# Optimization experiments

Hardware: AMD Instinct MI355X
Metric: run time of the kernel (lower is better)

Reference implementation:

```python
import jax, jax.numpy as jnp
import numpy as np

DIM, DEPTH, MULT = 512, 3, 4
E = 2 ** DEPTH            # 8 experts
HID = MULT * DIM          # 2048
B, S = 4, 1024


def setup_inputs() -> dict:
    key = jax.random.key(0)
    ks = jax.random.split(key, 7)
    sd = 1.0 / np.sqrt(DIM)
    sh = 1.0 / np.sqrt(HID)
    return {
        "x": jax.random.normal(ks[0], (B, S, DIM), dtype=jnp.float32),
        "rw": jax.random.normal(ks[1], (E - 1, DIM), dtype=jnp.float32) * sd,
        "rb": jax.random.normal(ks[2], (E - 1,), dtype=jnp.float32) * sd,
        "w1": jax.random.normal(ks[3], (E, DIM, HID), dtype=jnp.float32) * sd,
        "b1": jax.random.normal(ks[4], (E, HID), dtype=jnp.float32) * sd,
        "w2": jax.random.normal(ks[5], (E, HID, DIM), dtype=jnp.float32) * sh,
        "b2": jax.random.normal(ks[6], (E, DIM), dtype=jnp.float32) * sh,
    }


def _leaf_probs(flat_x, rw, rb):
    # Binary-tree soft routing: level d has 2**d routers at offset 2**d - 1.
    n_tok = flat_x.shape[0]
    leaf = jnp.ones((n_tok, 1), dtype=flat_x.dtype)
    for d in range(DEPTH):
        off, n = 2 ** d - 1, 2 ** d
        logits = flat_x @ rw[off:off + n].T + rb[off:off + n]   # [N, n]
        p = jax.nn.sigmoid(logits)
        # child probs: left = 1-p, right = p
        leaf = (leaf[:, :, None] * jnp.stack([1.0 - p, p], axis=2)).reshape(n_tok, 2 * n)
    return leaf  # [N, E]


def reference(x, rw, rb, w1, b1, w2, b2):
    b, s, dim = x.shape
    flat_x = x.reshape(b * s, dim)                               # [N, D]
    leaf_probs = _leaf_probs(flat_x, rw, rb)                     # [N, E]
    # Dense evaluation of all experts (soft-routing training path).
    h = jnp.einsum('nd,edh->neh', flat_x, w1) + b1[None]         # [N, E, H]
    h = jax.nn.gelu(h, approximate=False)                        # torch nn.GELU (erf)
    y = jnp.einsum('neh,ehd->ned', h, w2) + b2[None]             # [N, E, D]
    out = jnp.einsum('ned,ne->nd', y, leaf_probs)                # [N, D]
    return out.reshape(b, s, dim)
```

## Files before the change

kernel.cpp:

```cpp
#include <hip/hip_runtime.h>
#include <hip/hip_bf16.h>
#include <hip/hip_fp16.h>

#define DIM 512
#define HID 2048
#define NE 8
#define NTOK 4096

typedef _Float16 v8h __attribute__((ext_vector_type(8)));
typedef float v16f __attribute__((ext_vector_type(16)));

__device__ __forceinline__ void load16(const void* g, void* l) {
  __builtin_amdgcn_global_load_lds(
      (const __attribute__((address_space(1))) unsigned int*)g,
      (__attribute__((address_space(3))) unsigned int*)l, 16, 0, 0);
}

__device__ __forceinline__ float gelu_fast(float v) {
  float v2 = v * v;
  float u = v * __builtin_fmaf(0.07135481627f, v2, 1.5957691216f);
  float t = __expf(-u);
  return v * __builtin_amdgcn_rcpf(1.0f + t);
}

__global__ __launch_bounds__(256) void pre_kernel(const float* __restrict__ x,
                                                  const float* __restrict__ rw,
                                                  const float* __restrict__ rb,
                                                  const float* __restrict__ b2,
                                                  const float* __restrict__ w1,
                                                  const float* __restrict__ w2,
                                                  float* __restrict__ leaf,
                                                  _Float16* __restrict__ xh,
                                                  float* __restrict__ out,
                                                  _Float16* __restrict__ w1t,
                                                  _Float16* __restrict__ w2t) {
  __shared__ _Float16 tl[32][516];
  if (blockIdx.x < 1024) {
    const int lane = threadIdx.x & 63;
    const int wave = threadIdx.x >> 6;
    const int n = (blockIdx.x << 2) + wave;
    const float4* xv = (const float4*)(x + (size_t)n * DIM);
    const float4 x0 = xv[lane * 2], x1 = xv[lane * 2 + 1];
    v8h o;
    o[0] = (_Float16)x0.x; o[1] = (_Float16)x0.y; o[2] = (_Float16)x0.z; o[3] = (_Float16)x0.w;
    o[4] = (_Float16)x1.x; o[5] = (_Float16)x1.y; o[6] = (_Float16)x1.z; o[7] = (_Float16)x1.w;
    *(v8h*)(xh + (size_t)n * DIM + lane * 8) = o;
    float logits[7];
#pragma unroll
    for (int rr = 0; rr < 7; ++rr) {
      const float4* wv = (const float4*)(rw + rr * DIM);
      const float4 w0 = wv[lane * 2], w1v = wv[lane * 2 + 1];
      float s = x0.x * w0.x + x0.y * w0.y + x0.z * w0.z + x0.w * w0.w +
                x1.x * w1v.x + x1.y * w1v.y + x1.z * w1v.z + x1.w * w1v.w;
#pragma unroll
      for (int o2 = 32; o2; o2 >>= 1) s += __shfl_xor(s, o2, 64);
      logits[rr] = s + rb[rr];
    }
    const int eidx = lane & 7;
    const float p0 = 1.f / (1.f + __expf(-logits[0]));
    float f = ((eidx >> 2) & 1) ? p0 : 1.f - p0;
    const float p1 = 1.f / (1.f + __expf(-logits[1 + (eidx >> 2)]));
    f *= ((eidx >> 1) & 1) ? p1 : 1.f - p1;
    const float p2 = 1.f / (1.f + __expf(-logits[3 + (eidx >> 1)]));
    f *= (eidx & 1) ? p2 : 1.f - p2;
    if (lane < NE) leaf[(size_t)n * NE + lane] = f;
    float le[NE];
#pragma unroll
    for (int e = 0; e < NE; ++e) le[e] = __shfl(f, e, 64);
    float4 a0 = {0.f, 0.f, 0.f, 0.f}, a1 = {0.f, 0.f, 0.f, 0.f};
#pragma unroll
    for (int e = 0; e < NE; ++e) {
      const float4* bv = (const float4*)(b2 + (size_t)e * DIM + lane * 8);
      const float4 u0 = bv[0], u1 = bv[1];
      a0.x += le[e] * u0.x; a0.y += le[e] * u0.y; a0.z += le[e] * u0.z; a0.w += le[e] * u0.w;
      a1.x += le[e] * u1.x; a1.y += le[e] * u1.y; a1.z += le[e] * u1.z; a1.w += le[e] * u1.w;
    }
    float4* op = (float4*)(out + (size_t)n * DIM + lane * 8);
    op[0] = a0; op[1] = a1;
  } else {
    int t = blockIdx.x - 1024;
    const float* in;
    _Float16* outp;
    int C, Rk, kt, ct, e;
    if (t < 512) {
      in = w1; outp = w1t; C = HID; Rk = DIM;
      e = t >> 6; const int rem = t & 63; kt = rem & 15; ct = rem >> 4;
    } else {
      t -= 512;
      in = w2; outp = w2t; C = DIM; Rk = HID;
      e = t >> 6; kt = t & 63; ct = 0;
    }
    const int kb0 = kt << 5, cb0 = ct << 9;
    const size_t ebase = (size_t)e * Rk * C;
    const int tid = threadIdx.x;
#pragma unroll
    for (int i = 0; i < 16; ++i) {
      const int idx = (i << 8) + tid;
      const int row = idx >> 7, c4 = idx & 127;
      const float4 v = *(const float4*)(in + ebase + (size_t)(kb0 + row) * C + cb0 + (c4 << 2));
      _Float16* lp = &tl[row][c4 << 2];
      lp[0] = (_Float16)v.x; lp[1] = (_Float16)v.y; lp[2] = (_Float16)v.z; lp[3] = (_Float16)v.w;
    }
    __syncthreads();
#pragma unroll
    for (int h = 0; h < 2; ++h) {
      const int n = (h << 8) + tid;
      v8h o[4];
#pragma unroll
      for (int g = 0; g < 4; ++g)
#pragma unroll
        for (int u = 0; u < 8; ++u)
          o[g][u] = tl[(g << 3) + u][n];
      v8h* dst = (v8h*)(outp + ebase + (size_t)(cb0 + n) * Rk + kb0);
#pragma unroll
      for (int g = 0; g < 4; ++g) dst[g] = o[g];
    }
  }
}


__global__ __launch_bounds__(256, 3) void gemm1_kernel(const _Float16* __restrict__ xh,
                                                       const _Float16* __restrict__ w1t,
                                                       const float* __restrict__ b1,
                                                       const float* __restrict__ leaf,
                                                       _Float16* __restrict__ H) {
  const int bx = blockIdx.x;
  const int e = bx & 7;
  const int t = bx >> 3;
  const int mt = t & 31;
  const int nt = t >> 5;
  const int m0 = mt << 7, n0 = nt << 7;

  __shared__ alignas(16) _Float16 As[128 * 64];
  __shared__ alignas(16) _Float16 Bs[128 * 64];

  const int tid = threadIdx.x;
  const int lane = tid & 63;
  const int wave = tid >> 6;
  const int wm = wave >> 1, wn = wave & 1;
  const int c = lane & 31, h2 = lane >> 5;
  const int cx = c & 7;

  const int strow = tid >> 3;
  const int c8 = (tid & 7) ^ (strow & 7);
  const _Float16* pa[4];
  const _Float16* pb[4];
  _Float16* la[4];
  _Float16* lb[4];
#pragma unroll
  for (int i = 0; i < 4; ++i) {
    pa[i] = xh + (size_t)(m0 + strow + 32 * i) * DIM + (c8 << 3);
    la[i] = As + tid * 8 + i * 2048;
    pb[i] = w1t + ((size_t)e * HID + n0 + strow + 32 * i) * DIM + (c8 << 3);
    lb[i] = Bs + tid * 8 + i * 2048;
  }
  const _Float16* fA[2];
  const _Float16* fB[2];
#pragma unroll
  for (int i = 0; i < 2; ++i) fA[i] = As + ((wm << 6) + (i << 5) + c) * 64;
#pragma unroll
  for (int j = 0; j < 2; ++j) fB[j] = Bs + ((wn << 6) + (j << 5) + c) * 64;

  v16f acc[2][2];
#pragma unroll
  for (int i = 0; i < 2; ++i)
#pragma unroll
    for (int j = 0; j < 2; ++j)
      acc[i][j] = v16f{0.f,0.f,0.f,0.f,0.f,0.f,0.f,0.f,0.f,0.f,0.f,0.f,0.f,0.f,0.f,0.f};

#pragma unroll
  for (int kk = 0; kk < 8; ++kk) {
#pragma unroll
    for (int i = 0; i < 4; ++i) load16(pa[i] + kk * 64, la[i]);
#pragma unroll
    for (int i = 0; i < 4; ++i) load16(pb[i] + kk * 64, lb[i]);
    __syncthreads();
#pragma unroll
    for (int ks = 0; ks < 4; ++ks) {
      const int so = ((((ks << 1) + h2) ^ cx) << 3);
      v8h a[2], b[2];
#pragma unroll
      for (int i = 0; i < 2; ++i) a[i] = *(const v8h*)(fA[i] + so);
#pragma unroll
      for (int j = 0; j < 2; ++j) b[j] = *(const v8h*)(fB[j] + so);
#pragma unroll
      for (int i = 0; i < 2; ++i)
#pragma unroll
        for (int j = 0; j < 2; ++j)
          acc[i][j] = __builtin_amdgcn_mfma_f32_32x32x16_f16(a[i], b[j], acc[i][j], 0, 0, 0);
    }
    __syncthreads();
  }

  const float* b1e = b1 + (size_t)e * HID;
  _Float16* He = H + (size_t)e * NTOK * HID;
  const int colb = n0 + (wn << 6) + c;
  const float bias0 = b1e[colb];
  const float bias1 = b1e[colb + 32];
#pragma unroll
  for (int i = 0; i < 2; ++i) {
    const int rb0 = m0 + (wm << 6) + (i << 5) + (h2 << 2);
#pragma unroll
    for (int rg = 0; rg < 4; ++rg) {
#pragma unroll
      for (int rr = 0; rr < 4; ++rr) {
        const int row = rb0 + (rg << 3) + rr;
        const int reg = (rg << 2) + rr;
        const float p = leaf[(size_t)row * NE + e];
        _Float16* hp = He + (size_t)row * HID + colb;
        hp[0]  = (_Float16)(p * gelu_fast(acc[i][0][reg] + bias0));
        hp[32] = (_Float16)(p * gelu_fast(acc[i][1][reg] + bias1));
      }
    }
  }
}

__global__ __launch_bounds__(256, 3) void gemm2_kernel(const _Float16* __restrict__ H,
                                                       const _Float16* __restrict__ w2t,
                                                       float* __restrict__ out) {
  const int bx = blockIdx.x;
  const int e = bx & 7;
  const int dt = (bx >> 3) & 3;
  const int mt = bx >> 5;
  const int m0 = mt << 7, d0 = dt << 7;

  __shared__ alignas(16) _Float16 As[128 * 64];
  __shared__ alignas(16) _Float16 Bs[128 * 64];

  const int tid = threadIdx.x;
  const int lane = tid & 63;
  const int wave = tid >> 6;
  const int wm = wave >> 1, wn = wave & 1;
  const int c = lane & 31, h2 = lane >> 5;
  const int cx = c & 7;

  const int strow = tid >> 3;
  const int c8 = (tid & 7) ^ (strow & 7);
  const _Float16* pa[4];
  const _Float16* pb[4];
  _Float16* la[4];
  _Float16* lb[4];
#pragma unroll
  for (int i = 0; i < 4; ++i) {
    pa[i] = H + ((size_t)e * NTOK + m0 + strow + 32 * i) * HID + (c8 << 3);
    la[i] = As + tid * 8 + i * 2048;
    pb[i] = w2t + ((size_t)e * DIM + d0 + strow + 32 * i) * HID + (c8 << 3);
    lb[i] = Bs + tid * 8 + i * 2048;
  }
  const _Float16* fA[2];
  const _Float16* fB[2];
#pragma unroll
  for (int i = 0; i < 2; ++i) fA[i] = As + ((wm << 6) + (i << 5) + c) * 64;
#pragma unroll
  for (int j = 0; j < 2; ++j) fB[j] = Bs + ((wn << 6) + (j << 5) + c) * 64;

  v16f acc[2][2];
#pragma unroll
  for (int i = 0; i < 2; ++i)
#pragma unroll
    for (int j = 0; j < 2; ++j)
      acc[i][j] = v16f{0.f,0.f,0.f,0.f,0.f,0.f,0.f,0.f,0.f,0.f,0.f,0.f,0.f,0.f,0.f,0.f};

  for (int ko = 0; ko < 4; ++ko) {
#pragma unroll
    for (int u = 0; u < 8; ++u) {
#pragma unroll
      for (int i = 0; i < 4; ++i) load16(pa[i] + u * 64, la[i]);
#pragma unroll
      for (int i = 0; i < 4; ++i) load16(pb[i] + u * 64, lb[i]);
      __syncthreads();
#pragma unroll
      for (int ks = 0; ks < 4; ++ks) {
        const int so = ((((ks << 1) + h2) ^ cx) << 3);
        v8h a[2], b[2];
#pragma unroll
        for (int i = 0; i < 2; ++i) a[i] = *(const v8h*)(fA[i] + so);
#pragma unroll
        for (int j = 0; j < 2; ++j) b[j] = *(const v8h*)(fB[j] + so);
#pragma unroll
        for (int i = 0; i < 2; ++i)
#pragma unroll
          for (int j = 0; j < 2; ++j)
            acc[i][j] = __builtin_amdgcn_mfma_f32_32x32x16_f16(a[i], b[j], acc[i][j], 0, 0, 0);
      }
      __syncthreads();
    }
#pragma unroll
    for (int i = 0; i < 4; ++i) { pa[i] += 512; pb[i] += 512; }
  }

#pragma unroll
  for (int i = 0; i < 2; ++i) {
    const int rb0 = m0 + (wm << 6) + (i << 5) + (h2 << 2);
#pragma unroll
    for (int rg = 0; rg < 4; ++rg) {
#pragma unroll
      for (int rr = 0; rr < 4; ++rr) {
        const int row = rb0 + (rg << 3) + rr;
        const int reg = (rg << 2) + rr;
        float* op = out + (size_t)row * DIM + d0 + (wn << 6) + c;
        atomicAdd(op, acc[i][0][reg]);
        atomicAdd(op + 32, acc[i][1][reg]);
      }
    }
  }
}

extern "C" void kernel_launch(void* const* d_in, const int* in_sizes, int n_in,
                              void* d_out, int out_size, void* d_ws, size_t ws_size,
                              hipStream_t stream) {
  const float* x  = (const float*)d_in[0];
  const float* rw = (const float*)d_in[1];
  const float* rb = (const float*)d_in[2];
  const float* w1 = (const float*)d_in[3];
  const float* b1 = (const float*)d_in[4];
  const float* w2 = (const float*)d_in[5];
  const float* b2 = (const float*)d_in[6];
  float* out = (float*)d_out;

  char* ws = (char*)d_ws;
  const size_t xh_bytes   = (size_t)NTOK * DIM * 2;
  const size_t w1t_bytes  = (size_t)NE * HID * DIM * 2;
  const size_t w2t_bytes  = (size_t)NE * DIM * HID * 2;
  const size_t leaf_bytes = (size_t)NTOK * NE * 4;
  const size_t H_bytes    = (size_t)NE * NTOK * HID * 2;
  _Float16* xh   = (_Float16*)(ws);
  _Float16* w1t  = (_Float16*)(ws + xh_bytes);
  _Float16* w2t  = (_Float16*)(ws + xh_bytes + w1t_bytes);
  float*    leaf = (float*)(ws + xh_bytes + w1t_bytes + w2t_bytes);
  _Float16* Hbuf = (_Float16*)(ws + xh_bytes + w1t_bytes + w2t_bytes + leaf_bytes);
  if (ws_size < xh_bytes + w1t_bytes + w2t_bytes + leaf_bytes + H_bytes) return;

  pre_kernel<<<2048, 256, 0, stream>>>(x, rw, rb, b2, w1, w2, leaf, xh, out, w1t, w2t);
  gemm1_kernel<<<4096, 256, 0, stream>>>(xh, w1t, b1, leaf, Hbuf);
  gemm2_kernel<<<1024, 256, 0, stream>>>(Hbuf, w2t, out);
}
```

Before: 340.7 us.

## Double-buffer GEMM LDS tiles and split routing from weight transpose

Both GEMM kernels now use two LDS buffers: the global-to-LDS loads for the next K-slice are issued before the MFMAs on the current slice, with one barrier per step instead of two. This is meant to hide load latency behind compute. MFMA sections are bracketed by s_setprio, and occupancy hints drop from 3 to 2 blocks per SM because LDS use doubles. The pre-kernel is split into a routing kernel and a separate weight-transpose kernel, which uses a transposed LDS layout with 4-row float4 reads and vectorised half stores; this adds one kernel launch.

```diff
diff --git a/kernel.cpp b/kernel.cpp
--- a/kernel.cpp
+++ b/kernel.cpp
@@ -8,6 +8,7 @@
 #define NTOK 4096
 
 typedef _Float16 v8h __attribute__((ext_vector_type(8)));
+typedef _Float16 v4h __attribute__((ext_vector_type(4)));
 typedef float v16f __attribute__((ext_vector_type(16)));
 
 __device__ __forceinline__ void load16(const void* g, void* l) {
@@ -23,103 +24,152 @@
   return v * __builtin_amdgcn_rcpf(1.0f + t);
 }
 
-__global__ __launch_bounds__(256) void pre_kernel(const float* __restrict__ x,
-                                                  const float* __restrict__ rw,
-                                                  const float* __restrict__ rb,
-                                                  const float* __restrict__ b2,
-                                                  const float* __restrict__ w1,
-                                                  const float* __restrict__ w2,
-                                                  float* __restrict__ leaf,
-                                                  _Float16* __restrict__ xh,
-                                                  float* __restrict__ out,
-                                                  _Float16* __restrict__ w1t,
-                                                  _Float16* __restrict__ w2t) {
-  __shared__ _Float16 tl[32][516];
-  if (blockIdx.x < 1024) {
-    const int lane = threadIdx.x & 63;
-    const int wave = threadIdx.x >> 6;
-    const int n = (blockIdx.x << 2) + wave;
-    const float4* xv = (const float4*)(x + (size_t)n * DIM);
-    const float4 x0 = xv[lane * 2], x1 = xv[lane * 2 + 1];
-    v8h o;
-    o[0] = (_Float16)x0.x; o[1] = (_Float16)x0.y; o[2] = (_Float16)x0.z; o[3] = (_Float16)x0.w;
-    o[4] = (_Float16)x1.x; o[5] = (_Float16)x1.y; o[6] = (_Float16)x1.z; o[7] = (_Float16)x1.w;
-    *(v8h*)(xh + (size_t)n * DIM + lane * 8) = o;
-    float logits[7];
-#pragma unroll
-    for (int rr = 0; rr < 7; ++rr) {
-      const float4* wv = (const float4*)(rw + rr * DIM);
-      const float4 w0 = wv[lane * 2], w1v = wv[lane * 2 + 1];
-      float s = x0.x * w0.x + x0.y * w0.y + x0.z * w0.z + x0.w * w0.w +
-                x1.x * w1v.x + x1.y * w1v.y + x1.z * w1v.z + x1.w * w1v.w;
-#pragma unroll
-      for (int o2 = 32; o2; o2 >>= 1) s += __shfl_xor(s, o2, 64);
-      logits[rr] = s + rb[rr];
-    }
-    const int eidx = lane & 7;
-    const float p0 = 1.f / (1.f + __expf(-logits[0]));
-    float f = ((eidx >> 2) & 1) ? p0 : 1.f - p0;
-    const float p1 = 1.f / (1.f + __expf(-logits[1 + (eidx >> 2)]));
-    f *= ((eidx >> 1) & 1) ? p1 : 1.f - p1;
-    const float p2 = 1.f / (1.f + __expf(-logits[3 + (eidx >> 1)]));
-    f *= (eidx & 1) ? p2 : 1.f - p2;
-    if (lane < NE) leaf[(size_t)n * NE + lane] = f;
-    float le[NE];
-#pragma unroll
-    for (int e = 0; e < NE; ++e) le[e] = __shfl(f, e, 64);
-    float4 a0 = {0.f, 0.f, 0.f, 0.f}, a1 = {0.f, 0.f, 0.f, 0.f};
-#pragma unroll
-    for (int e = 0; e < NE; ++e) {
-      const float4* bv = (const float4*)(b2 + (size_t)e * DIM + lane * 8);
-      const float4 u0 = bv[0], u1 = bv[1];
-      a0.x += le[e] * u0.x; a0.y += le[e] * u0.y; a0.z += le[e] * u0.z; a0.w += le[e] * u0.w;
-      a1.x += le[e] * u1.x; a1.y += le[e] * u1.y; a1.z += le[e] * u1.z; a1.w += le[e] * u1.w;
-    }
-    float4* op = (float4*)(out + (size_t)n * DIM + lane * 8);
-    op[0] = a0; op[1] = a1;
+__global__ __launch_bounds__(256) void route_kernel(const float* __restrict__ x,
+                                                    const float* __restrict__ rw,
+                                                    const float* __restrict__ rb,
+                                                    const float* __restrict__ b2,
+                                                    float* __restrict__ leaf,
+                                                    _Float16* __restrict__ xh,
+                                                    float* __restrict__ out) {
+  const int lane = threadIdx.x & 63;
+  const int wave = threadIdx.x >> 6;
+  const int n = (blockIdx.x << 2) + wave;
+  const float4* xv = (const float4*)(x + (size_t)n * DIM);
+  const float4 x0 = xv[lane * 2], x1 = xv[lane * 2 + 1];
+  v8h o;
+  o[0] = (_Float16)x0.x; o[1] = (_Float16)x0.y; o[2] = (_Float16)x0.z; o[3] = (_Float16)x0.w;
+  o[4] = (_Float16)x1.x; o[5] = (_Float16)x1.y; o[6] = (_Float16)x1.z; o[7] = (_Float16)x1.w;
+  *(v8h*)(xh + (size_t)n * DIM + lane * 8) = o;
+  float logits[7];
+#pragma unroll
+  for (int rr = 0; rr < 7; ++rr) {
+    const float4* wv = (const float4*)(rw + rr * DIM);
+    const float4 w0 = wv[lane * 2], w1v = wv[lane * 2 + 1];
+    float s = x0.x * w0.x + x0.y * w0.y + x0.z * w0.z + x0.w * w0.w +
+              x1.x * w1v.x + x1.y * w1v.y + x1.z * w1v.z + x1.w * w1v.w;
+#pragma unroll
+    for (int o2 = 32; o2; o2 >>= 1) s += __shfl_xor(s, o2, 64);
+    logits[rr] = s + rb[rr];
+  }
+  const int eidx = lane & 7;
+  const float p0 = 1.f / (1.f + __expf(-logits[0]));
+  float f = ((eidx >> 2) & 1) ? p0 : 1.f - p0;
+  const float p1 = 1.f / (1.f + __expf(-logits[1 + (eidx >> 2)]));
+  f *= ((eidx >> 1) & 1) ? p1 : 1.f - p1;
+  const float p2 = 1.f / (1.f + __expf(-logits[3 + (eidx >> 1)]));
+  f *= (eidx & 1) ? p2 : 1.f - p2;
+  if (lane < NE) leaf[(size_t)n * NE + lane] = f;
+  float le[NE];
+#pragma unroll
+  for (int e = 0; e < NE; ++e) le[e] = __shfl(f, e, 64);
+  float4 a0 = {0.f, 0.f, 0.f, 0.f}, a1 = {0.f, 0.f, 0.f, 0.f};
+#pragma unroll
+  for (int e = 0; e < NE; ++e) {
+    const float4* bv = (const float4*)(b2 + (size_t)e * DIM + lane * 8);
+    const float4 u0 = bv[0], u1 = bv[1];
+    a0.x += le[e] * u0.x; a0.y += le[e] * u0.y; a0.z += le[e] * u0.z; a0.w += le[e] * u0.w;
+    a1.x += le[e] * u1.x; a1.y += le[e] * u1.y; a1.z += le[e] * u1.z; a1.w += le[e] * u1.w;
+  }
+  float4* op = (float4*)(out + (size_t)n * DIM + lane * 8);
+  op[0] = a0; op[1] = a1;
+}
+
+__global__ __launch_bounds__(256) void trans_kernel(const float* __restrict__ w1,
+                                                    const float* __restrict__ w2,
+                                                    _Float16* __restrict__ w1t,
+                                                    _Float16* __restrict__ w2t) {
+  __shared__ _Float16 tlT[256][36];
+  int b = blockIdx.x;
+  const float* in;
+  _Float16* outp;
+  int C, Rk, kt, ct, e;
+  if (b < 1024) {
+    in = w1; outp = w1t; C = HID; Rk = DIM;
+    e = b >> 7; const int rem = b & 127; kt = rem & 15; ct = rem >> 4;
   } else {
-    int t = blockIdx.x - 1024;
-    const float* in;
-    _Float16* outp;
-    int C, Rk, kt, ct, e;
-    if (t < 512) {
-      in = w1; outp = w1t; C = HID; Rk = DIM;
-      e = t >> 6; const int rem = t & 63; kt = rem & 15; ct = rem >> 4;
-    } else {
-      t -= 512;
-      in = w2; outp = w2t; C = DIM; Rk = HID;
-      e = t >> 6; kt = t & 63; ct = 0;
-    }
-    const int kb0 = kt << 5, cb0 = ct << 9;
-    const size_t ebase = (size_t)e * Rk * C;
-    const int tid = threadIdx.x;
-#pragma unroll
-    for (int i = 0; i < 16; ++i) {
-      const int idx = (i << 8) + tid;
-      const int row = idx >> 7, c4 = idx & 127;
-      const float4 v = *(const float4*)(in + ebase + (size_t)(kb0 + row) * C + cb0 + (c4 << 2));
-      _Float16* lp = &tl[row][c4 << 2];
-      lp[0] = (_Float16)v.x; lp[1] = (_Float16)v.y; lp[2] = (_Float16)v.z; lp[3] = (_Float16)v.w;
-    }
-    __syncthreads();
-#pragma unroll
-    for (int h = 0; h < 2; ++h) {
-      const int n = (h << 8) + tid;
-      v8h o[4];
-#pragma unroll
-      for (int g = 0; g < 4; ++g)
-#pragma unroll
-        for (int u = 0; u < 8; ++u)
-          o[g][u] = tl[(g << 3) + u][n];
-      v8h* dst = (v8h*)(outp + ebase + (size_t)(cb0 + n) * Rk + kb0);
-#pragma unroll
-      for (int g = 0; g < 4; ++g) dst[g] = o[g];
-    }
-  }
-}
-
-
-__global__ __launch_bounds__(256, 3) void gemm1_kernel(const _Float16* __restrict__ xh,
+    b -= 1024;
+    in = w2; outp = w2t; C = DIM; Rk = HID;
+    e = b >> 7; const int rem = b & 127; kt = rem & 63; ct = rem >> 6;
+  }
+  const int k0 = kt << 5, c0 = ct << 8;
+  const size_t ebase = (size_t)e * Rk * C;
+  const int tid = threadIdx.x;
+#pragma unroll
+  for (int it = 0; it < 2; ++it) {
+    const int mb = (it << 8) + tid;
+    const int rg = mb >> 6, cq = mb & 63;
+    const float* sp = in + ebase + (size_t)(k0 + (rg << 2)) * C + c0 + (cq << 2);
+    const float4 r0 = *(const float4*)(sp);
+    const float4 r1 = *(const float4*)(sp + C);
+    const float4 r2 = *(const float4*)(sp + 2 * C);
+    const float4 r3 = *(const float4*)(sp + 3 * C);
+    const int cc = cq << 2, rr = rg << 2;
+    v4h t0 = {(_Float16)r0.x, (_Float16)r1.x, (_Float16)r2.x, (_Float16)r3.x};
+    v4h t1 = {(_Float16)r0.y, (_Float16)r1.y, (_Float16)r2.y, (_Float16)r3.y};
+    v4h t2 = {(_Float16)r0.z, (_Float16)r1.z, (_Float16)r2.z, (_Float16)r3.z};
+    v4h t3 = {(_Float16)r0.w, (_Float16)r1.w, (_Float16)r2.w, (_Float16)r3.w};
+    *(v4h*)&tlT[cc + 0][rr] = t0;
+    *(v4h*)&tlT[cc + 1][rr] = t1;
+    *(v4h*)&tlT[cc + 2][rr] = t2;
+    *(v4h*)&tlT[cc + 3][rr] = t3;
+  }
+  __syncthreads();
+  v8h ov[4];
+#pragma unroll
+  for (int g = 0; g < 4; ++g) {
+    const v4h lo = *(const v4h*)&tlT[tid][g * 8];
+    const v4h hi = *(const v4h*)&tlT[tid][g * 8 + 4];
+    ov[g][0] = lo[0]; ov[g][1] = lo[1]; ov[g][2] = lo[2]; ov[g][3] = lo[3];
+    ov[g][4] = hi[0]; ov[g][5] = hi[1]; ov[g][6] = hi[2]; ov[g][7] = hi[3];
+  }
+  _Float16* dp = outp + ebase + (size_t)(c0 + tid) * Rk + k0;
+#pragma unroll
+  for (int g = 0; g < 4; ++g) *(v8h*)(dp + g * 8) = ov[g];
+}
+
+
+#define WAIT0() asm volatile("s_waitcnt vmcnt(0)" ::: "memory")
+#define BARF()                                                                \
+  {                                                                           \
+    __builtin_amdgcn_s_barrier();                                             \
+    asm volatile("" ::: "memory");                                            \
+  }
+
+#define GSTAGE(BOF, KO)                                                       \
+  {                                                                           \
+    _Pragma("unroll") for (int i = 0; i < 4; ++i)                             \
+        load16(pa[i] + (KO), la[i] + (BOF));                                  \
+    _Pragma("unroll") for (int i = 0; i < 4; ++i)                             \
+        load16(pb[i] + (KO), lb[i] + (BOF));                                  \
+  }
+
+#define GCOMPUTE(BOF)                                                         \
+  {                                                                           \
+    v8h a[2][4], b[2][4];                                                     \
+    _Pragma("unroll") for (int ks = 0; ks < 4; ++ks) {                        \
+      const int so = (BOF) + ((((ks << 1) + h2) ^ cx) << 3);                  \
+      a[0][ks] = *(const v8h*)(fA[0] + so);                                   \
+      a[1][ks] = *(const v8h*)(fA[1] + so);                                   \
+      b[0][ks] = *(const v8h*)(fB[0] + so);                                   \
+      b[1][ks] = *(const v8h*)(fB[1] + so);                                   \
+    }                                                                         \
+    __builtin_amdgcn_s_setprio(1);                                            \
+    _Pragma("unroll") for (int ks = 0; ks < 4; ++ks)                          \
+      _Pragma("unroll") for (int i = 0; i < 2; ++i)                           \
+        _Pragma("unroll") for (int j = 0; j < 2; ++j)                         \
+          acc[i][j] = __builtin_amdgcn_mfma_f32_32x32x16_f16(a[i][ks], b[j][ks], acc[i][j], 0, 0, 0); \
+    __builtin_amdgcn_s_setprio(0);                                            \
+  }
+
+#define GITER(BUFC, BUFS, KO)                                                 \
+  {                                                                           \
+    GSTAGE(BUFS, KO);                                                         \
+    GCOMPUTE(BUFC);                                                           \
+    WAIT0();                                                                  \
+    BARF();                                                                   \
+  }
+
+__global__ __launch_bounds__(256, 2) void gemm1_kernel(const _Float16* __restrict__ xh,
                                                        const _Float16* __restrict__ w1t,
                                                        const float* __restrict__ b1,
                                                        const float* __restrict__ leaf,
@@ -131,8 +181,8 @@
   const int nt = t >> 5;
   const int m0 = mt << 7, n0 = nt << 7;
 
-  __shared__ alignas(16) _Float16 As[128 * 64];
-  __shared__ alignas(16) _Float16 Bs[128 * 64];
+  __shared__ alignas(16) _Float16 As[2 * 128 * 64];
+  __shared__ alignas(16) _Float16 Bs[2 * 128 * 64];
 
   const int tid = threadIdx.x;
   const int lane = tid & 63;
@@ -168,29 +218,16 @@
     for (int j = 0; j < 2; ++j)
       acc[i][j] = v16f{0.f,0.f,0.f,0.f,0.f,0.f,0.f,0.f,0.f,0.f,0.f,0.f,0.f,0.f,0.f,0.f};
 
-#pragma unroll
-  for (int kk = 0; kk < 8; ++kk) {
-#pragma unroll
-    for (int i = 0; i < 4; ++i) load16(pa[i] + kk * 64, la[i]);
-#pragma unroll
-    for (int i = 0; i < 4; ++i) load16(pb[i] + kk * 64, lb[i]);
-    __syncthreads();
-#pragma unroll
-    for (int ks = 0; ks < 4; ++ks) {
-      const int so = ((((ks << 1) + h2) ^ cx) << 3);
-      v8h a[2], b[2];
-#pragma unroll
-      for (int i = 0; i < 2; ++i) a[i] = *(const v8h*)(fA[i] + so);
-#pragma unroll
-      for (int j = 0; j < 2; ++j) b[j] = *(const v8h*)(fB[j] + so);
-#pragma unroll
-      for (int i = 0; i < 2; ++i)
-#pragma unroll
-        for (int j = 0; j < 2; ++j)
-          acc[i][j] = __builtin_amdgcn_mfma_f32_32x32x16_f16(a[i], b[j], acc[i][j], 0, 0, 0);
-    }
-    __syncthreads();
-  }
+  GSTAGE(0, 0);
+  WAIT0(); BARF();
+  GITER(0, 8192, 64);
+  GITER(8192, 0, 128);
+  GITER(0, 8192, 192);
+  GITER(8192, 0, 256);
+  GITER(0, 8192, 320);
+  GITER(8192, 0, 384);
+  GITER(0, 8192, 448);
+  GCOMPUTE(8192);
 
   const float* b1e = b1 + (size_t)e * HID;
   _Float16* He = H + (size_t)e * NTOK * HID;
@@ -215,7 +252,7 @@
   }
 }
 
-__global__ __launch_bounds__(256, 3) void gemm2_kernel(const _Float16* __restrict__ H,
+__global__ __launch_bounds__(256, 2) void gemm2_kernel(const _Float16* __restrict__ H,
                                                        const _Float16* __restrict__ w2t,
                                                        float* __restrict__ out) {
   const int bx = blockIdx.x;
@@ -224,8 +261,8 @@
   const int mt = bx >> 5;
   const int m0 = mt << 7, d0 = dt << 7;
 
-  __shared__ alignas(16) _Float16 As[128 * 64];
-  __shared__ alignas(16) _Float16 Bs[128 * 64];
+  __shared__ alignas(16) _Float16 As[2 * 128 * 64];
+  __shared__ alignas(16) _Float16 Bs[2 * 128 * 64];
 
   const int tid = threadIdx.x;
   const int lane = tid & 63;
@@ -261,33 +298,16 @@
     for (int j = 0; j < 2; ++j)
       acc[i][j] = v16f{0.f,0.f,0.f,0.f,0.f,0.f,0.f,0.f,0.f,0.f,0.f,0.f,0.f,0.f,0.f,0.f};
 
-  for (int ko = 0; ko < 4; ++ko) {
-#pragma unroll
-    for (int u = 0; u < 8; ++u) {
-#pragma unroll
-      for (int i = 0; i < 4; ++i) load16(pa[i] + u * 64, la[i]);
-#pragma unroll
-      for (int i = 0; i < 4; ++i) load16(pb[i] + u * 64, lb[i]);
-      __syncthreads();
-#pragma unroll
-      for (int ks = 0; ks < 4; ++ks) {
-        const int so = ((((ks << 1) + h2) ^ cx) << 3);
-        v8h a[2], b[2];
-#pragma unroll
-        for (int i = 0; i < 2; ++i) a[i] = *(const v8h*)(fA[i] + so);
-#pragma unroll
-        for (int j = 0; j < 2; ++j) b[j] = *(const v8h*)(fB[j] + so);
-#pragma unroll
-        for (int i = 0; i < 2; ++i)
-#pragma unroll
-          for (int j = 0; j < 2; ++j)
-            acc[i][j] = __builtin_amdgcn_mfma_f32_32x32x16_f16(a[i], b[j], acc[i][j], 0, 0, 0);
-      }
-      __syncthreads();
-    }
-#pragma unroll
-    for (int i = 0; i < 4; ++i) { pa[i] += 512; pb[i] += 512; }
-  }
+  GSTAGE(0, 0);
+  WAIT0(); BARF();
+  for (int ko = 0; ko < 15; ++ko) {
+    GITER(0, 8192, 64);
+    GITER(8192, 0, 128);
+#pragma unroll
+    for (int i = 0; i < 4; ++i) { pa[i] += 128; pb[i] += 128; }
+  }
+  GITER(0, 8192, 64);
+  GCOMPUTE(8192);
 
 #pragma unroll
   for (int i = 0; i < 2; ++i) {
@@ -331,7 +351,8 @@
   _Float16* Hbuf = (_Float16*)(ws + xh_bytes + w1t_bytes + w2t_bytes + leaf_bytes);
   if (ws_size < xh_bytes + w1t_bytes + w2t_bytes + leaf_bytes + H_bytes) return;
 
-  pre_kernel<<<2048, 256, 0, stream>>>(x, rw, rb, b2, w1, w2, leaf, xh, out, w1t, w2t);
+  route_kernel<<<1024, 256, 0, stream>>>(x, rw, rb, b2, leaf, xh, out);
+  trans_kernel<<<2048, 256, 0, stream>>>(w1, w2, w1t, w2t);
   gemm1_kernel<<<4096, 256, 0, stream>>>(xh, w1t, b1, leaf, Hbuf);
   gemm2_kernel<<<1024, 256, 0, stream>>>(Hbuf, w2t, out);
 }
```

Result: slower. 364.8 us (+7.1%).
